# Optimization experiments

Hardware: AMD Instinct MI355X
Metric: run time of the kernel (lower is better)

The kernel has to match this reference:

```python
import jax, jax.numpy as jnp
import numpy as np

N, E, C, S = 30000, 480000, 256, 4
T_EVO = 0.1        # evolution_time
MAX_EIG = 0.5      # max_eigenval in create_ultra_stable_hamiltonian
MAX_NORM = 0.01    # max_norm in ultra_stable_matrix_exp
MAX_TERMS = 4
LN_EPS = 1e-5


def _build_subgraphs(edge_index, n, s):
    """Emulates the per-node k_hop=1 BFS (capped at max_subgraph_size=s) and the
    subgraph laplacian Hamiltonian build (edge_weight=0.1, self-loops added).
    Pure structural preprocessing: integer/constant w.r.t. all float params."""
    src = np.asarray(edge_index[0], dtype=np.int64)
    dst = np.asarray(edge_index[1], dtype=np.int64)
    loops = np.arange(n, dtype=np.int64)
    src = np.concatenate([src, loops]); dst = np.concatenate([dst, loops])
    order = np.argsort(src, kind='stable')
    src_s, dst_s = src[order], dst[order]
    starts = np.searchsorted(src_s, np.arange(n))
    ends = np.searchsorted(src_s, np.arange(n) + 1)
    edge_set = set((src * n + dst).tolist())
    sub_nodes = np.zeros((n, s), dtype=np.int64)
    sub_mask = np.zeros((n, s), dtype=np.float32)
    H = np.zeros((n, s, s), dtype=np.float32)
    for i in range(n):
        nbrs = [i]
        for d in dst_s[starts[i]:ends[i]]:
            d = int(d)
            if d != i and d not in nbrs:
                nbrs.append(d)
                if len(nbrs) == s:
                    break
        m = len(nbrs)
        sub_nodes[i, :m] = nbrs
        sub_nodes[i, m:] = i          # pad with center (masked out below)
        sub_mask[i, :m] = 1.0
        A = np.zeros((s, s), dtype=np.float32)
        for a in range(m):
            ka = nbrs[a] * n
            for b in range(m):
                if (ka + nbrs[b]) in edge_set:
                    A[a, b] = 1.0
        deg = np.maximum(A.sum(axis=1), 1e-6)   # degree(row), clamped like torch
        H[i] = np.diag(deg) - 0.1 * A           # laplacian with edge_weight=0.1
    return sub_nodes, sub_mask, H


def _mat_fro(M):
    return jnp.sqrt(jnp.sum(jnp.abs(M) ** 2, axis=(-2, -1)))


def _unitary_from_H(sub_H):
    """ultra_stable_matrix_exp, batched over N tiny [S,S] Hamiltonians.
    The torch .item() norm/eigenvalue rescales detach gradients, so treating this
    whole block as parameter-independent (it is: H is structural) is faithful."""
    Hc = sub_H.astype(jnp.complex64)
    ev = jnp.linalg.eigvals(Hc)                              # [N,S] (CPU op)
    mx = jnp.max(ev.real, axis=-1)
    Hc = Hc * jnp.where(mx > MAX_EIG, MAX_EIG / mx, 1.0)[:, None, None]
    hn = _mat_fro(Hc)
    Hc = Hc * jnp.where(hn > MAX_NORM, MAX_NORM / hn, 1.0)[:, None, None]
    A = (-1j) * Hc * (T_EVO * 0.1)                           # scaled_H
    I = jnp.eye(S, dtype=jnp.complex64)
    U = jnp.broadcast_to(I, Hc.shape)
    term = U
    for k in range(1, MAX_TERMS + 1):
        term = jnp.matmul(term, A) / k
        tn = _mat_fro(term)
        term = term * jnp.where(tn > 0.1, 0.1 / tn, 1.0)[:, None, None]
        U = U + term
    err = _mat_fro(jnp.matmul(U, jnp.conj(jnp.swapaxes(U, -1, -2))) - I)
    U = jnp.where((err > 0.1)[:, None, None], I + A * 0.01, U)
    return U


def _cplx_linear(xr, xi, wr, wi, br, bi):
    xr = jnp.clip(xr, -10.0, 10.0); xi = jnp.clip(xi, -10.0, 10.0)
    re = xr @ wr.T - xi @ wi.T + br
    im = xr @ wi.T + xi @ wr.T + bi
    return re + 1j * im


def _cln(z, w, b, eps=LN_EPS):
    # UltraStableComplexLayerNorm, training-mode batch stats over dim 0
    mag = jnp.clip(jnp.sqrt(z.real ** 2 + z.imag ** 2 + eps), eps, 1000.0)
    mean = mag.mean(0)
    var = mag.var(0)
    nm = (mag - mean) / (jnp.sqrt(var + eps) + eps)
    sm = jnp.clip(nm * jnp.abs(w) + b, eps, 10.0)
    ph = jnp.arctan2(jnp.clip(z.imag, -1e6, 1e6), jnp.clip(z.real, -1e6, 1e6) + 1e-10)
    return sm * jnp.cos(ph) + 1j * (sm * jnp.sin(ph))


def _crelu(z, leak=0.01, mx=5.0):
    r = jnp.clip(z.real, -mx, mx); i = jnp.clip(z.imag, -mx, mx)
    return jnp.where(r > 0, r, leak * r) + 1j * jnp.where(i > 0, i, leak * i)


def setup_inputs() -> dict:
    key = jax.random.key(0)
    k1, k2, k3, k4 = jax.random.split(key, 4)
    x = jax.random.normal(k1, (N, C), dtype=jnp.float32)
    edge_index = jax.random.randint(k2, (2, E), 0, N, dtype=jnp.int64)
    sub_nodes, sub_mask, sub_H = _build_subgraphs(np.asarray(edge_index), N, S)
    std = np.sqrt(0.5 / C).astype(np.float32)
    w_real = jax.random.normal(k3, (C, C), dtype=jnp.float32) * std
    w_imag = jax.random.normal(k4, (C, C), dtype=jnp.float32) * std
    return {
        'x': x,
        'edge_index': edge_index,
        'sub_nodes': jnp.asarray(sub_nodes),
        'sub_mask': jnp.asarray(sub_mask),
        'sub_H': jnp.asarray(sub_H),
        'w_real': w_real,
        'w_imag': w_imag,
        'b_real': jnp.zeros((C,), jnp.float32),
        'b_imag': jnp.zeros((C,), jnp.float32),
        'ln_weight': jnp.full((C,), 0.1, jnp.float32),
        'ln_bias': jnp.zeros((C,), jnp.float32),
        'evolution_scale': jnp.asarray(0.1, jnp.float32),
    }


def reference(x, edge_index, sub_nodes, sub_mask, sub_H,
              w_real, w_imag, b_real, b_imag, ln_weight, ln_bias,
              evolution_scale):
    # complex linear (input is real -> imag part zero, matching torch.complex(x, 0*x))
    h = _cplx_linear(x, jnp.zeros_like(x), w_real, w_imag, b_real, b_imag)  # [N,C] c64
    U = _unitary_from_H(sub_H)                                              # [N,S,S]
    sub_x = h[sub_nodes] * sub_mask[..., None]                              # [N,S,C]
    # center node is slot 0 of each subgraph -> take row 0 of U @ sub_x
    evolved = jnp.einsum('ns,nsc->nc', U[:, 0, :], sub_x)
    out = evolved * evolution_scale + x.astype(jnp.complex64)  # residual (in==out)
    out = _cln(out, ln_weight, ln_bias)
    out = _crelu(out)
    # dropout is eval-mode identity
    return jnp.concatenate([out.real, out.imag], axis=-1)      # [N, 2C] float32
```

## Files before the change

kernel.cpp:

```cpp
#include <hip/hip_runtime.h>
#include <stdint.h>

#define N_NODES 30000
#define NC 256

typedef _Float16 f16x8 __attribute__((ext_vector_type(8)));
typedef _Float16 f16x4 __attribute__((ext_vector_type(4)));
typedef _Float16 f16x2 __attribute__((ext_vector_type(2)));
typedef float f32x4 __attribute__((ext_vector_type(4)));

__global__ void k_conv_x(const float* __restrict__ x, _Float16* __restrict__ xb) {
    int i = (blockIdx.x * 256 + threadIdx.x) * 4;
    float4 v = *reinterpret_cast<const float4*>(x + i);
    f16x4 o;
    o[0] = (_Float16)fminf(fmaxf(v.x, -10.f), 10.f);
    o[1] = (_Float16)fminf(fmaxf(v.y, -10.f), 10.f);
    o[2] = (_Float16)fminf(fmaxf(v.z, -10.f), 10.f);
    o[3] = (_Float16)fminf(fmaxf(v.w, -10.f), 10.f);
    *reinterpret_cast<f16x4*>(xb + i) = o;
}

__global__ void k_conv_w(const float* __restrict__ wr, const float* __restrict__ wi,
                         _Float16* __restrict__ Wb) {
    int i = (blockIdx.x * 256 + threadIdx.x) * 4;
    const float* src = (i < NC * NC) ? (wr + i) : (wi + (i - NC * NC));
    float4 v = *reinterpret_cast<const float4*>(src);
    f16x4 o;
    o[0] = (_Float16)v.x; o[1] = (_Float16)v.y;
    o[2] = (_Float16)v.z; o[3] = (_Float16)v.w;
    *reinterpret_cast<f16x4*>(Wb + i) = o;
}

__global__ __launch_bounds__(256) void k_gemm(
    const _Float16* __restrict__ A, const _Float16* __restrict__ B,
    const float* __restrict__ br, const float* __restrict__ bi,
    _Float16* __restrict__ H)
{
    int bid = blockIdx.x;
    int bm = bid >> 2, bn = bid & 3;
    int tid = threadIdx.x;
    int lane = tid & 63, wave = tid >> 6;
    int quad = lane >> 4, l16 = lane & 15;
    int wm = wave >> 1, wn = wave & 1;
    int row0 = bm * 128 + wm * 64;
    int col0 = bn * 128 + wn * 64;

    const _Float16* ap[4];
    const _Float16* bp[4];
#pragma unroll
    for (int mi = 0; mi < 4; mi++) {
        int r = row0 + mi * 16 + l16;
        if (r >= N_NODES) r = N_NODES - 1;
        ap[mi] = A + r * NC + quad * 8;
    }
#pragma unroll
    for (int ni = 0; ni < 4; ni++)
        bp[ni] = B + (col0 + ni * 16 + l16) * NC + quad * 8;

    f32x4 acc[4][4] = {};
    for (int k = 0; k < NC; k += 32) {
        f16x8 af[4], bfr[4];
#pragma unroll
        for (int mi = 0; mi < 4; mi++) af[mi] = *reinterpret_cast<const f16x8*>(ap[mi] + k);
#pragma unroll
        for (int ni = 0; ni < 4; ni++) bfr[ni] = *reinterpret_cast<const f16x8*>(bp[ni] + k);
#pragma unroll
        for (int mi = 0; mi < 4; mi++)
#pragma unroll
            for (int ni = 0; ni < 4; ni++)
                acc[mi][ni] = __builtin_amdgcn_mfma_f32_16x16x32_f16(
                    af[mi], bfr[ni], acc[mi][ni], 0, 0, 0);
    }
#pragma unroll
    for (int ni = 0; ni < 4; ni++) {
        int col = col0 + ni * 16 + l16;
        float bias = (col < NC) ? br[col] : bi[col - NC];
        int cc = (col < NC) ? (col * 2) : ((col - NC) * 2 + 1);
#pragma unroll
        for (int mi = 0; mi < 4; mi++) {
            int rowb = row0 + mi * 16 + quad * 4;
#pragma unroll
            for (int r = 0; r < 4; r++) {
                int row = rowb + r;
                if (row < N_NODES) H[row * 512 + cc] = (_Float16)(acc[mi][ni][r] + bias);
            }
        }
    }
}

#define NPB 30
__global__ __launch_bounds__(256) void k_evolve(
    const float* __restrict__ x, const int* __restrict__ sub_nodes,
    const float* __restrict__ sub_mask, const float* __restrict__ subH,
    const _Float16* __restrict__ h, const float* __restrict__ escp,
    float* __restrict__ outz, _Float16* __restrict__ zbuf, int use_f16,
    float* __restrict__ ssum, float* __restrict__ ssumsq)
{
    __shared__ int   s_nodes[NPB][4];
    __shared__ float s_g[NPB][4];
    __shared__ float s_m0[NPB];
    int tid = threadIdx.x;
    int base = blockIdx.x * NPB;
    if (tid < NPB) {
        int node = base + tid;
        float fr = 0.f;
#pragma unroll
        for (int t = 0; t < 16; t++) { float v = subH[node * 16 + t]; fr += v * v; }
        float coef = 1e-4f * rsqrtf(fr);
#pragma unroll
        for (int s = 0; s < 4; s++) {
            s_g[tid][s]     = coef * subH[node * 16 + s] * sub_mask[node * 4 + s];
            s_nodes[tid][s] = sub_nodes[node * 4 + s];
        }
        s_m0[tid] = sub_mask[node * 4];
    }
    __syncthreads();
    float esc = *escp;
    float lsum = 0.f, lsq = 0.f;
    for (int j = 0; j < NPB; j++) {
        int node = base + j;
        float evr = 0.f, evi = 0.f;
#pragma unroll
        for (int s = 0; s < 4; s++) {
            int ns = s_nodes[j][s];
            float g = s_g[j][s];
            f16x2 v = *reinterpret_cast<const f16x2*>(h + ns * 512 + tid * 2);
            float hr = (float)v[0], hi = (float)v[1];
            evr += g * hi;
            evi -= g * hr;
            if (s == 0) { float m0 = s_m0[j]; evr += m0 * hr; evi += m0 * hi; }
        }
        float xr = x[node * NC + tid];
        float outr = fmaf(esc, evr, xr);
        float outi = esc * evi;
        if (use_f16) {
            f16x2 o; o[0] = (_Float16)outr; o[1] = (_Float16)outi;
            *reinterpret_cast<f16x2*>(zbuf + node * 512 + tid * 2) = o;
        } else {
            outz[node * 512 + tid] = outr;
            outz[node * 512 + 256 + tid] = outi;
        }
        float mag = sqrtf(fmaf(outr, outr, fmaf(outi, outi, 1e-5f)));
        mag = fminf(fmaxf(mag, 1e-5f), 1000.f);
        lsum += mag;
        lsq = fmaf(mag, mag, lsq);
    }
    atomicAdd(&ssum[tid], lsum);
    atomicAdd(&ssumsq[tid], lsq);
}

__global__ void k_stats(const float* __restrict__ ssum, const float* __restrict__ ssumsq,
                        const float* __restrict__ lnw, const float* __restrict__ lnb,
                        float* __restrict__ stA, float* __restrict__ stB)
{
    int c = threadIdx.x;
    const float invN = 1.0f / (float)N_NODES;
    float mean = ssum[c] * invN;
    float var = fmaxf(ssumsq[c] * invN - mean * mean, 0.f);
    float denom = sqrtf(var + 1e-5f) + 1e-5f;
    float a = fabsf(lnw[c]) / denom;
    stA[c] = a;
    stB[c] = lnb[c] - mean * a;
}

__global__ __launch_bounds__(256) void k_norm(
    float* __restrict__ out, const _Float16* __restrict__ zbuf, int use_f16,
    const float* __restrict__ stA, const float* __restrict__ stB)
{
    int tid = threadIdx.x;
    int node = blockIdx.x * 4 + (tid >> 6);
    int c0 = (tid & 63) * 4;
    float re[4], im[4];
    if (use_f16) {
        f16x8 z = *reinterpret_cast<const f16x8*>(zbuf + node * 512 + c0 * 2);
#pragma unroll
        for (int e = 0; e < 4; e++) { re[e] = (float)z[2 * e]; im[e] = (float)z[2 * e + 1]; }
    } else {
        float4 r4 = *reinterpret_cast<const float4*>(out + node * 512 + c0);
        float4 i4 = *reinterpret_cast<const float4*>(out + node * 512 + 256 + c0);
        re[0] = r4.x; re[1] = r4.y; re[2] = r4.z; re[3] = r4.w;
        im[0] = i4.x; im[1] = i4.y; im[2] = i4.z; im[3] = i4.w;
    }
    float4 a4 = *reinterpret_cast<const float4*>(stA + c0);
    float4 b4 = *reinterpret_cast<const float4*>(stB + c0);
    float A[4] = {a4.x, a4.y, a4.z, a4.w};
    float B[4] = {b4.x, b4.y, b4.z, b4.w};
    float orr[4], oii[4];
#pragma unroll
    for (int e = 0; e < 4; e++) {
        float r = re[e], i = im[e];
        float mag = sqrtf(fmaf(r, r, fmaf(i, i, 1e-5f)));
        mag = fminf(fmaxf(mag, 1e-5f), 1000.f);
        float sm = fmaf(mag, A[e], B[e]);
        sm = fminf(fmaxf(sm, 1e-5f), 10.0f);
        float px = fminf(fmaxf(r, -1e6f), 1e6f) + 1e-10f;
        float py = fminf(fmaxf(i, -1e6f), 1e6f);
        float r2 = fmaf(px, px, py * py);
        float inv = rsqrtf(r2);
        float zr = sm * px * inv, zi = sm * py * inv;
        zr = fminf(fmaxf(zr, -5.f), 5.f);
        zi = fminf(fmaxf(zi, -5.f), 5.f);
        orr[e] = zr > 0.f ? zr : 0.01f * zr;
        oii[e] = zi > 0.f ? zi : 0.01f * zi;
    }
    *reinterpret_cast<float4*>(out + node * 512 + c0) =
        make_float4(orr[0], orr[1], orr[2], orr[3]);
    *reinterpret_cast<float4*>(out + node * 512 + 256 + c0) =
        make_float4(oii[0], oii[1], oii[2], oii[3]);
}

extern "C" void kernel_launch(void* const* d_in, const int* in_sizes, int n_in,
                              void* d_out, int out_size, void* d_ws, size_t ws_size,
                              hipStream_t stream) {
    const float* x        = (const float*)d_in[0];
    const int*   sub_nodes = (const int*)d_in[2];
    const float* sub_mask  = (const float*)d_in[3];
    const float* subH      = (const float*)d_in[4];
    const float* wr  = (const float*)d_in[5];
    const float* wi  = (const float*)d_in[6];
    const float* br  = (const float*)d_in[7];
    const float* bi  = (const float*)d_in[8];
    const float* lnw = (const float*)d_in[9];
    const float* lnb = (const float*)d_in[10];
    const float* esc = (const float*)d_in[11];
    float* out = (float*)d_out;

    char* ws = (char*)d_ws;
    const size_t XB_OFF   = 0;
    const size_t WB_OFF   = 15360000;
    const size_t H_OFF    = 15622144;
    const size_t STAT_OFF = 46342144;
    const size_t ZB_OFF   = 46346240;
    const size_t WS_NEED_F16 = ZB_OFF + 30720000;
    _Float16* xb = (_Float16*)(ws + XB_OFF);
    _Float16* Wb = (_Float16*)(ws + WB_OFF);
    _Float16* h  = (_Float16*)(ws + H_OFF);
    float* ssum   = (float*)(ws + STAT_OFF);
    float* ssumsq = (float*)(ws + STAT_OFF + 1024);
    float* stA    = (float*)(ws + STAT_OFF + 2048);
    float* stB    = (float*)(ws + STAT_OFF + 3072);
    _Float16* zbuf = (_Float16*)(ws + ZB_OFF);
    int use_f16 = (ws_size >= WS_NEED_F16) ? 1 : 0;

    hipMemsetAsync(ssum, 0, 2048, stream);
    hipLaunchKernelGGL(k_conv_x, dim3(7500), dim3(256), 0, stream, x, xb);
    hipLaunchKernelGGL(k_conv_w, dim3(128), dim3(256), 0, stream, wr, wi, Wb);
    hipLaunchKernelGGL(k_gemm, dim3(235 * 4), dim3(256), 0, stream, xb, Wb, br, bi, h);
    hipLaunchKernelGGL(k_evolve, dim3(1000), dim3(256), 0, stream,
                       x, sub_nodes, sub_mask, subH, h, esc, out, zbuf, use_f16,
                       ssum, ssumsq);
    hipLaunchKernelGGL(k_stats, dim3(1), dim3(256), 0, stream,
                       ssum, ssumsq, lnw, lnb, stA, stB);
    hipLaunchKernelGGL(k_norm, dim3(7500), dim3(256), 0, stream,
                       out, zbuf, use_f16, stA, stB);
}
```

Before: 224.9 us.

## Fuse x conversion into GEMM, fold stats into norm, prefetch K tiles

Removes the separate fp32-to-fp16 conversion kernel for x: the GEMM now reads fp32 x directly, then clamps and converts it in registers. It also removes the single-block stats kernel by recomputing per-channel mean/variance coefficients inside k_norm. Each GEMM wave now covers matching real and imag output columns, and the K loop double-buffers register fragments so loads overlap MFMAs. This drops two launches and one write-plus-read pass over x, at the cost of wider fp32 A loads in the GEMM, extra register pressure, and redundant stats math per thread.

```diff
diff --git a/kernel.cpp b/kernel.cpp
--- a/kernel.cpp
+++ b/kernel.cpp
@@ -8,17 +8,6 @@
 typedef _Float16 f16x4 __attribute__((ext_vector_type(4)));
 typedef _Float16 f16x2 __attribute__((ext_vector_type(2)));
 typedef float f32x4 __attribute__((ext_vector_type(4)));
-
-__global__ void k_conv_x(const float* __restrict__ x, _Float16* __restrict__ xb) {
-    int i = (blockIdx.x * 256 + threadIdx.x) * 4;
-    float4 v = *reinterpret_cast<const float4*>(x + i);
-    f16x4 o;
-    o[0] = (_Float16)fminf(fmaxf(v.x, -10.f), 10.f);
-    o[1] = (_Float16)fminf(fmaxf(v.y, -10.f), 10.f);
-    o[2] = (_Float16)fminf(fmaxf(v.z, -10.f), 10.f);
-    o[3] = (_Float16)fminf(fmaxf(v.w, -10.f), 10.f);
-    *reinterpret_cast<f16x4*>(xb + i) = o;
-}
 
 __global__ void k_conv_w(const float* __restrict__ wr, const float* __restrict__ wi,
                          _Float16* __restrict__ Wb) {
@@ -32,7 +21,7 @@
 }
 
 __global__ __launch_bounds__(256) void k_gemm(
-    const _Float16* __restrict__ A, const _Float16* __restrict__ B,
+    const float* __restrict__ X, const _Float16* __restrict__ B,
     const float* __restrict__ br, const float* __restrict__ bi,
     _Float16* __restrict__ H)
 {
@@ -43,39 +32,70 @@
     int quad = lane >> 4, l16 = lane & 15;
     int wm = wave >> 1, wn = wave & 1;
     int row0 = bm * 128 + wm * 64;
-    int col0 = bn * 128 + wn * 64;
-
-    const _Float16* ap[4];
+    int cbase = bn * 64;
+    int brow0 = (wn ? 256 : 0) + cbase;
+
+    const float* xp[4];
     const _Float16* bp[4];
 #pragma unroll
     for (int mi = 0; mi < 4; mi++) {
         int r = row0 + mi * 16 + l16;
         if (r >= N_NODES) r = N_NODES - 1;
-        ap[mi] = A + r * NC + quad * 8;
+        xp[mi] = X + r * NC + quad * 8;
     }
 #pragma unroll
     for (int ni = 0; ni < 4; ni++)
-        bp[ni] = B + (col0 + ni * 16 + l16) * NC + quad * 8;
+        bp[ni] = B + (brow0 + ni * 16 + l16) * NC + quad * 8;
 
     f32x4 acc[4][4] = {};
-    for (int k = 0; k < NC; k += 32) {
-        f16x8 af[4], bfr[4];
-#pragma unroll
-        for (int mi = 0; mi < 4; mi++) af[mi] = *reinterpret_cast<const f16x8*>(ap[mi] + k);
-#pragma unroll
-        for (int ni = 0; ni < 4; ni++) bfr[ni] = *reinterpret_cast<const f16x8*>(bp[ni] + k);
+    f16x8 a0[4], b0[4], a1[4], b1[4];
+
+    auto loadA = [&](f16x8* dst, int k) {
+#pragma unroll
+        for (int mi = 0; mi < 4; mi++) {
+            float4 u = *reinterpret_cast<const float4*>(xp[mi] + k);
+            float4 v = *reinterpret_cast<const float4*>(xp[mi] + k + 4);
+            f16x8 t;
+            t[0] = (_Float16)fminf(fmaxf(u.x, -10.f), 10.f);
+            t[1] = (_Float16)fminf(fmaxf(u.y, -10.f), 10.f);
+            t[2] = (_Float16)fminf(fmaxf(u.z, -10.f), 10.f);
+            t[3] = (_Float16)fminf(fmaxf(u.w, -10.f), 10.f);
+            t[4] = (_Float16)fminf(fmaxf(v.x, -10.f), 10.f);
+            t[5] = (_Float16)fminf(fmaxf(v.y, -10.f), 10.f);
+            t[6] = (_Float16)fminf(fmaxf(v.z, -10.f), 10.f);
+            t[7] = (_Float16)fminf(fmaxf(v.w, -10.f), 10.f);
+            dst[mi] = t;
+        }
+    };
+    auto loadB = [&](f16x8* dst, int k) {
+#pragma unroll
+        for (int ni = 0; ni < 4; ni++)
+            dst[ni] = *reinterpret_cast<const f16x8*>(bp[ni] + k);
+    };
+    auto domfma = [&](f16x8* a, f16x8* b) {
 #pragma unroll
         for (int mi = 0; mi < 4; mi++)
 #pragma unroll
             for (int ni = 0; ni < 4; ni++)
                 acc[mi][ni] = __builtin_amdgcn_mfma_f32_16x16x32_f16(
-                    af[mi], bfr[ni], acc[mi][ni], 0, 0, 0);
-    }
+                    a[mi], b[ni], acc[mi][ni], 0, 0, 0);
+    };
+
+    loadA(a0, 0); loadB(b0, 0);
+#pragma unroll
+    for (int kk = 0; kk < NC; kk += 64) {
+        if (kk + 32 < NC) { loadA(a1, kk + 32); loadB(b1, kk + 32); }
+        domfma(a0, b0);
+        if (kk + 64 < NC) { loadA(a0, kk + 64); loadB(b0, kk + 64); }
+        domfma(a1, b1);
+    }
+
+    const float* bias_p = wn ? bi : br;
 #pragma unroll
     for (int ni = 0; ni < 4; ni++) {
-        int col = col0 + ni * 16 + l16;
-        float bias = (col < NC) ? br[col] : bi[col - NC];
-        int cc = (col < NC) ? (col * 2) : ((col - NC) * 2 + 1);
+        int c = cbase + ni * 16 + l16;
+        float bias = bias_p[c];
+        int cc = 2 * c + wn;
 #pragma unroll
         for (int mi = 0; mi < 4; mi++) {
             int rowb = row0 + mi * 16 + quad * 4;
@@ -149,23 +169,10 @@
     atomicAdd(&ssumsq[tid], lsq);
 }
 
-__global__ void k_stats(const float* __restrict__ ssum, const float* __restrict__ ssumsq,
-                        const float* __restrict__ lnw, const float* __restrict__ lnb,
-                        float* __restrict__ stA, float* __restrict__ stB)
-{
-    int c = threadIdx.x;
-    const float invN = 1.0f / (float)N_NODES;
-    float mean = ssum[c] * invN;
-    float var = fmaxf(ssumsq[c] * invN - mean * mean, 0.f);
-    float denom = sqrtf(var + 1e-5f) + 1e-5f;
-    float a = fabsf(lnw[c]) / denom;
-    stA[c] = a;
-    stB[c] = lnb[c] - mean * a;
-}
-
 __global__ __launch_bounds__(256) void k_norm(
     float* __restrict__ out, const _Float16* __restrict__ zbuf, int use_f16,
-    const float* __restrict__ stA, const float* __restrict__ stB)
+    const float* __restrict__ ssum, const float* __restrict__ ssumsq,
+    const float* __restrict__ lnw, const float* __restrict__ lnb)
 {
     int tid = threadIdx.x;
     int node = blockIdx.x * 4 + (tid >> 6);
@@ -181,17 +188,27 @@
         re[0] = r4.x; re[1] = r4.y; re[2] = r4.z; re[3] = r4.w;
         im[0] = i4.x; im[1] = i4.y; im[2] = i4.z; im[3] = i4.w;
     }
-    float4 a4 = *reinterpret_cast<const float4*>(stA + c0);
-    float4 b4 = *reinterpret_cast<const float4*>(stB + c0);
-    float A[4] = {a4.x, a4.y, a4.z, a4.w};
-    float B[4] = {b4.x, b4.y, b4.z, b4.w};
+    float4 s4 = *reinterpret_cast<const float4*>(ssum + c0);
+    float4 q4 = *reinterpret_cast<const float4*>(ssumsq + c0);
+    float4 w4 = *reinterpret_cast<const float4*>(lnw + c0);
+    float4 lb4 = *reinterpret_cast<const float4*>(lnb + c0);
+    float S[4] = {s4.x, s4.y, s4.z, s4.w};
+    float Q[4] = {q4.x, q4.y, q4.z, q4.w};
+    float W[4] = {w4.x, w4.y, w4.z, w4.w};
+    float L[4] = {lb4.x, lb4.y, lb4.z, lb4.w};
+    const float invN = 1.0f / (float)N_NODES;
     float orr[4], oii[4];
 #pragma unroll
     for (int e = 0; e < 4; e++) {
+        float mean = S[e] * invN;
+        float var = fmaxf(Q[e] * invN - mean * mean, 0.f);
+        float denom = sqrtf(var + 1e-5f) + 1e-5f;
+        float A = fabsf(W[e]) / denom;
+        float Bc = L[e] - mean * A;
         float r = re[e], i = im[e];
         float mag = sqrtf(fmaf(r, r, fmaf(i, i, 1e-5f)));
         mag = fminf(fmaxf(mag, 1e-5f), 1000.f);
-        float sm = fmaf(mag, A[e], B[e]);
+        float sm = fmaf(mag, A, Bc);
         sm = fminf(fmaxf(sm, 1e-5f), 10.0f);
         float px = fminf(fmaxf(r, -1e6f), 1e6f) + 1e-10f;
         float py = fminf(fmaxf(i, -1e6f), 1e6f);
@@ -226,31 +243,24 @@
     float* out = (float*)d_out;
 
     char* ws = (char*)d_ws;
-    const size_t XB_OFF   = 0;
-    const size_t WB_OFF   = 15360000;
-    const size_t H_OFF    = 15622144;
-    const size_t STAT_OFF = 46342144;
-    const size_t ZB_OFF   = 46346240;
+    const size_t WB_OFF   = 0;
+    const size_t H_OFF    = 262144;
+    const size_t STAT_OFF = 30982144;
+    const size_t ZB_OFF   = 30986240;
     const size_t WS_NEED_F16 = ZB_OFF + 30720000;
-    _Float16* xb = (_Float16*)(ws + XB_OFF);
     _Float16* Wb = (_Float16*)(ws + WB_OFF);
     _Float16* h  = (_Float16*)(ws + H_OFF);
     float* ssum   = (float*)(ws + STAT_OFF);
     float* ssumsq = (float*)(ws + STAT_OFF + 1024);
-    float* stA    = (float*)(ws + STAT_OFF + 2048);
-    float* stB    = (float*)(ws + STAT_OFF + 3072);
     _Float16* zbuf = (_Float16*)(ws + ZB_OFF);
     int use_f16 = (ws_size >= WS_NEED_F16) ? 1 : 0;
 
     hipMemsetAsync(ssum, 0, 2048, stream);
-    hipLaunchKernelGGL(k_conv_x, dim3(7500), dim3(256), 0, stream, x, xb);
     hipLaunchKernelGGL(k_conv_w, dim3(128), dim3(256), 0, stream, wr, wi, Wb);
-    hipLaunchKernelGGL(k_gemm, dim3(235 * 4), dim3(256), 0, stream, xb, Wb, br, bi, h);
+    hipLaunchKernelGGL(k_gemm, dim3(235 * 4), dim3(256), 0, stream, x, Wb, br, bi, h);
     hipLaunchKernelGGL(k_evolve, dim3(1000), dim3(256), 0, stream,
                        x, sub_nodes, sub_mask, subH, h, esc, out, zbuf, use_f16,
                        ssum, ssumsq);
-    hipLaunchKernelGGL(k_stats, dim3(1), dim3(256), 0, stream,
-                       ssum, ssumsq, lnw, lnb, stA, stB);
     hipLaunchKernelGGL(k_norm, dim3(7500), dim3(256), 0, stream,
-                       out, zbuf, use_f16, stA, stB);
-}
+                       out, zbuf, use_f16, ssum, ssumsq, lnw, lnb);
+}
```

New measurement: 228.0 us. About the same (+1.4%).

## Keep A rows in registers across GEMM column tiles and fold stats into norm

Applied to the files above, without the earlier changes.

Each GEMM block now loads its full 64x256 A fragment into registers once and reuses it for two 64-column output chunks. B loads are double-buffered across k-steps, and the grid is halved to 470 blocks with a 2-blocks-per-CU launch bound. The single-block k_stats kernel is removed: k_norm now recomputes mean, variance and the scale/shift per channel inline, which saves one launch at the cost of redundant ALU work per thread. The large register footprint (32 f16x8 A fragments plus accumulators) risks spills or low occupancy.

```diff
diff --git a/kernel.cpp b/kernel.cpp
--- a/kernel.cpp
+++ b/kernel.cpp
@@ -31,58 +31,70 @@
     *reinterpret_cast<f16x4*>(Wb + i) = o;
 }
 
-__global__ __launch_bounds__(256) void k_gemm(
+__global__ __launch_bounds__(256, 2) void k_gemm(
     const _Float16* __restrict__ A, const _Float16* __restrict__ B,
     const float* __restrict__ br, const float* __restrict__ bi,
     _Float16* __restrict__ H)
 {
     int bid = blockIdx.x;
-    int bm = bid >> 2, bn = bid & 3;
+    int bm = bid >> 1, cs = bid & 1;
     int tid = threadIdx.x;
     int lane = tid & 63, wave = tid >> 6;
     int quad = lane >> 4, l16 = lane & 15;
     int wm = wave >> 1, wn = wave & 1;
     int row0 = bm * 128 + wm * 64;
-    int col0 = bn * 128 + wn * 64;
-
-    const _Float16* ap[4];
-    const _Float16* bp[4];
+
+    f16x8 af[4][8];
 #pragma unroll
     for (int mi = 0; mi < 4; mi++) {
         int r = row0 + mi * 16 + l16;
         if (r >= N_NODES) r = N_NODES - 1;
-        ap[mi] = A + r * NC + quad * 8;
-    }
-#pragma unroll
-    for (int ni = 0; ni < 4; ni++)
-        bp[ni] = B + (col0 + ni * 16 + l16) * NC + quad * 8;
-
-    f32x4 acc[4][4] = {};
-    for (int k = 0; k < NC; k += 32) {
-        f16x8 af[4], bfr[4];
-#pragma unroll
-        for (int mi = 0; mi < 4; mi++) af[mi] = *reinterpret_cast<const f16x8*>(ap[mi] + k);
-#pragma unroll
-        for (int ni = 0; ni < 4; ni++) bfr[ni] = *reinterpret_cast<const f16x8*>(bp[ni] + k);
-#pragma unroll
-        for (int mi = 0; mi < 4; mi++)
-#pragma unroll
-            for (int ni = 0; ni < 4; ni++)
-                acc[mi][ni] = __builtin_amdgcn_mfma_f32_16x16x32_f16(
-                    af[mi], bfr[ni], acc[mi][ni], 0, 0, 0);
-    }
-#pragma unroll
-    for (int ni = 0; ni < 4; ni++) {
-        int col = col0 + ni * 16 + l16;
-        float bias = (col < NC) ? br[col] : bi[col - NC];
-        int cc = (col < NC) ? (col * 2) : ((col - NC) * 2 + 1);
-#pragma unroll
-        for (int mi = 0; mi < 4; mi++) {
-            int rowb = row0 + mi * 16 + quad * 4;
-#pragma unroll
-            for (int r = 0; r < 4; r++) {
-                int row = rowb + r;
-                if (row < N_NODES) H[row * 512 + cc] = (_Float16)(acc[mi][ni][r] + bias);
+        const _Float16* ap = A + r * NC + quad * 8;
+#pragma unroll
+        for (int kc = 0; kc < 8; kc++)
+            af[mi][kc] = *reinterpret_cast<const f16x8*>(ap + kc * 32);
+    }
+
+    const float* bias_p = wn ? bi : br;
+#pragma unroll
+    for (int cn = 0; cn < 2; cn++) {
+        const _Float16* bbase = B + ((wn ? 256 : 0) + cs * 128 + cn * 64 + l16) * NC
+                                  + quad * 8;
+        f16x8 bb[2][4];
+#pragma unroll
+        for (int ni = 0; ni < 4; ni++)
+            bb[0][ni] = *reinterpret_cast<const f16x8*>(bbase + ni * 16 * NC);
+        f32x4 acc[4][4] = {};
+#pragma unroll
+        for (int kc = 0; kc < 8; kc++) {
+            int cur = kc & 1, nxt = cur ^ 1;
+            if (kc < 7) {
+#pragma unroll
+                for (int ni = 0; ni < 4; ni++)
+                    bb[nxt][ni] = *reinterpret_cast<const f16x8*>(
+                        bbase + ni * 16 * NC + (kc + 1) * 32);
+            }
+#pragma unroll
+            for (int mi = 0; mi < 4; mi++)
+#pragma unroll
+                for (int ni = 0; ni < 4; ni++)
+                    acc[mi][ni] = __builtin_amdgcn_mfma_f32_16x16x32_f16(
+                        af[mi][kc], bb[cur][ni], acc[mi][ni], 0, 0, 0);
+        }
+#pragma unroll
+        for (int ni = 0; ni < 4; ni++) {
+            int c = cs * 128 + cn * 64 + ni * 16 + l16;
+            float bias = bias_p[c];
+            int cc = 2 * c + wn;
+#pragma unroll
+            for (int mi = 0; mi < 4; mi++) {
+                int rowb = row0 + mi * 16 + quad * 4;
+#pragma unroll
+                for (int r = 0; r < 4; r++) {
+                    int row = rowb + r;
+                    if (row < N_NODES)
+                        H[row * 512 + cc] = (_Float16)(acc[mi][ni][r] + bias);
+                }
             }
         }
     }
@@ -149,23 +161,10 @@
     atomicAdd(&ssumsq[tid], lsq);
 }
 
-__global__ void k_stats(const float* __restrict__ ssum, const float* __restrict__ ssumsq,
-                        const float* __restrict__ lnw, const float* __restrict__ lnb,
-                        float* __restrict__ stA, float* __restrict__ stB)
-{
-    int c = threadIdx.x;
-    const float invN = 1.0f / (float)N_NODES;
-    float mean = ssum[c] * invN;
-    float var = fmaxf(ssumsq[c] * invN - mean * mean, 0.f);
-    float denom = sqrtf(var + 1e-5f) + 1e-5f;
-    float a = fabsf(lnw[c]) / denom;
-    stA[c] = a;
-    stB[c] = lnb[c] - mean * a;
-}
-
 __global__ __launch_bounds__(256) void k_norm(
     float* __restrict__ out, const _Float16* __restrict__ zbuf, int use_f16,
-    const float* __restrict__ stA, const float* __restrict__ stB)
+    const float* __restrict__ ssum, const float* __restrict__ ssumsq,
+    const float* __restrict__ lnw, const float* __restrict__ lnb)
 {
     int tid = threadIdx.x;
     int node = blockIdx.x * 4 + (tid >> 6);
@@ -181,17 +180,27 @@
         re[0] = r4.x; re[1] = r4.y; re[2] = r4.z; re[3] = r4.w;
         im[0] = i4.x; im[1] = i4.y; im[2] = i4.z; im[3] = i4.w;
     }
-    float4 a4 = *reinterpret_cast<const float4*>(stA + c0);
-    float4 b4 = *reinterpret_cast<const float4*>(stB + c0);
-    float A[4] = {a4.x, a4.y, a4.z, a4.w};
-    float B[4] = {b4.x, b4.y, b4.z, b4.w};
+    float4 s4 = *reinterpret_cast<const float4*>(ssum + c0);
+    float4 q4 = *reinterpret_cast<const float4*>(ssumsq + c0);
+    float4 w4 = *reinterpret_cast<const float4*>(lnw + c0);
+    float4 lb4 = *reinterpret_cast<const float4*>(lnb + c0);
+    float S[4] = {s4.x, s4.y, s4.z, s4.w};
+    float Q[4] = {q4.x, q4.y, q4.z, q4.w};
+    float W[4] = {w4.x, w4.y, w4.z, w4.w};
+    float L[4] = {lb4.x, lb4.y, lb4.z, lb4.w};
+    const float invN = 1.0f / (float)N_NODES;
     float orr[4], oii[4];
 #pragma unroll
     for (int e = 0; e < 4; e++) {
+        float mean = S[e] * invN;
+        float var = fmaxf(Q[e] * invN - mean * mean, 0.f);
+        float denom = sqrtf(var + 1e-5f) + 1e-5f;
+        float A = fabsf(W[e]) / denom;
+        float Bc = L[e] - mean * A;
         float r = re[e], i = im[e];
         float mag = sqrtf(fmaf(r, r, fmaf(i, i, 1e-5f)));
         mag = fminf(fmaxf(mag, 1e-5f), 1000.f);
-        float sm = fmaf(mag, A[e], B[e]);
+        float sm = fmaf(mag, A, Bc);
         sm = fminf(fmaxf(sm, 1e-5f), 10.0f);
         float px = fminf(fmaxf(r, -1e6f), 1e6f) + 1e-10f;
         float py = fminf(fmaxf(i, -1e6f), 1e6f);
@@ -237,20 +246,16 @@
     _Float16* h  = (_Float16*)(ws + H_OFF);
     float* ssum   = (float*)(ws + STAT_OFF);
     float* ssumsq = (float*)(ws + STAT_OFF + 1024);
-    float* stA    = (float*)(ws + STAT_OFF + 2048);
-    float* stB    = (float*)(ws + STAT_OFF + 3072);
     _Float16* zbuf = (_Float16*)(ws + ZB_OFF);
     int use_f16 = (ws_size >= WS_NEED_F16) ? 1 : 0;
 
     hipMemsetAsync(ssum, 0, 2048, stream);
     hipLaunchKernelGGL(k_conv_x, dim3(7500), dim3(256), 0, stream, x, xb);
     hipLaunchKernelGGL(k_conv_w, dim3(128), dim3(256), 0, stream, wr, wi, Wb);
-    hipLaunchKernelGGL(k_gemm, dim3(235 * 4), dim3(256), 0, stream, xb, Wb, br, bi, h);
+    hipLaunchKernelGGL(k_gemm, dim3(235 * 2), dim3(256), 0, stream, xb, Wb, br, bi, h);
     hipLaunchKernelGGL(k_evolve, dim3(1000), dim3(256), 0, stream,
                        x, sub_nodes, sub_mask, subH, h, esc, out, zbuf, use_f16,
                        ssum, ssumsq);
-    hipLaunchKernelGGL(k_stats, dim3(1), dim3(256), 0, stream,
-                       ssum, ssumsq, lnw, lnb, stA, stB);
     hipLaunchKernelGGL(k_norm, dim3(7500), dim3(256), 0, stream,
-                       out, zbuf, use_f16, stA, stB);
-}
+                       out, zbuf, use_f16, ssum, ssumsq, lnw, lnb);
+}
```

New measurement: 215.2 us. 1.05x faster.
